# Kernel optimization log

Hardware: AMD Instinct MI355X
Metric: run time of the kernel (lower is better)

## Reference

```python
import jax, jax.numpy as jnp
import numpy as np
from jax import lax

B, H, W, CIN, COUT, K, SDIM = 8, 256, 256, 128, 128, 3, 512


def setup_inputs() -> dict:
    key = jax.random.key(0)
    k1, k2, k3, k4, k5 = jax.random.split(key, 5)
    return {
        "x": jax.random.normal(k1, (B, H, W, CIN), dtype=jnp.float32),
        "style": jax.random.normal(k2, (B, SDIM), dtype=jnp.float32),
        "kernel": jax.random.normal(k3, (K, K, CIN, COUT), dtype=jnp.float32),
        "w_mod": jax.random.normal(k4, (SDIM, CIN), dtype=jnp.float32) / np.sqrt(SDIM),
        "b_mod": jnp.zeros((CIN,), dtype=jnp.float32),
        "noise_strength": jnp.zeros((1,), dtype=jnp.float32),
        "bias": jnp.zeros((COUT,), dtype=jnp.float32),
        "noise": jax.random.normal(k5, (B, H, W, 1), dtype=jnp.float32),
    }


def reference(x, style, kernel, w_mod, b_mod, noise_strength, bias, noise):
    kh, kw, cin, cout = kernel.shape
    # equalized-lr runtime coefficient
    he_std = 1.0 / jnp.sqrt(jnp.asarray(kh * kw * cin, jnp.float32))
    w = kernel * he_std  # [kh,kw,cin,cout]
    # style modulation (Dense with zero constant bias) + 1
    s = style @ w_mod + b_mod + 1.0  # [B, cin]
    # demodulate=True: normalize by global max-abs of style (as in source)
    s = s * (1.0 / jnp.max(jnp.abs(s)))
    # NOTE: source uses style[0] only -> single shared modulated weight
    w = w * s[0][None, None, :, None]
    d = lax.rsqrt(jnp.sum(jnp.square(w), axis=(0, 1, 2)) + 1e-8)  # [cout]
    w = w * d[None, None, None, :]
    # plain conv branch: NHWC, stride 1, SAME padding
    y = lax.conv_general_dilated(
        x, w, window_strides=(1, 1), padding="SAME",
        dimension_numbers=("NHWC", "HWIO", "NHWC"))
    # noise injection (noise_strength is zero-init, kept for faithfulness)
    y = y + noise * (noise_strength / 2.0)
    y = y + bias
    # lrelu(0.2) * sqrt(2)
    y = jnp.where(y >= 0, y, 0.2 * y) * jnp.sqrt(jnp.asarray(2.0, y.dtype))
    return y
```

## Files before the change

kernel.cpp:

```cpp
#include <hip/hip_runtime.h>
#include <hip/hip_bf16.h>

#define H 256
#define W 256
#define CIN 128
#define COUT 128
#define BATCH 8
#define LDA 136

typedef float f32x4 __attribute__((ext_vector_type(4)));
typedef short bf16x8 __attribute__((ext_vector_type(8)));

static __device__ __forceinline__ unsigned short f2bf(float f) {
    unsigned int x = __float_as_uint(f);
    unsigned int r = (x + 0x7fffu + ((x >> 16) & 1u)) >> 16;
    return (unsigned short)r;
}

__global__ __launch_bounds__(1024) void prep_kernel(
    const float* __restrict__ style, const float* __restrict__ kern,
    const float* __restrict__ w_mod, const float* __restrict__ b_mod,
    unsigned short* __restrict__ wprep)
{
    __shared__ float sbuf[1024];
    __shared__ float scaleArr[CIN];
    __shared__ float dArr[COUT];
    const int t = threadIdx.x;
    const int b = t >> 7;
    const int c = t & 127;

    float acc = 0.f;
    const float4* st4 = (const float4*)(style + b * 512);
    for (int k4 = 0; k4 < 128; ++k4) {
        float4 s4 = st4[k4];
        int k = k4 * 4;
        acc += s4.x * w_mod[(k + 0) * CIN + c];
        acc += s4.y * w_mod[(k + 1) * CIN + c];
        acc += s4.z * w_mod[(k + 2) * CIN + c];
        acc += s4.w * w_mod[(k + 3) * CIN + c];
    }
    float sval = acc + b_mod[c] + 1.0f;

    sbuf[t] = fabsf(sval);
    __syncthreads();
    for (int off = 512; off > 0; off >>= 1) {
        if (t < off) sbuf[t] = fmaxf(sbuf[t], sbuf[t + off]);
        __syncthreads();
    }
    float invmax = 1.0f / sbuf[0];
    const float he_std = 1.0f / sqrtf(1152.0f);
    if (t < CIN) scaleArr[t] = sval * invmax * he_std;
    __syncthreads();

    {
        const int co = t & 127;
        const int slice = t >> 7;
        float ss = 0.f;
        for (int j = 0; j < 144; ++j) {
            int i = slice * 144 + j;
            int ci = i & 127;
            float wv = kern[i * 128 + co] * scaleArr[ci];
            ss += wv * wv;
        }
        sbuf[t] = ss;
        __syncthreads();
        if (t < 128) {
            float sum = 0.f;
            for (int sl = 0; sl < 8; ++sl) sum += sbuf[sl * 128 + t];
            dArr[t] = rsqrtf(sum + 1e-8f);
        }
        __syncthreads();
    }

    for (int u = t; u < 9 * 4 * 8 * 64; u += 1024) {
        int lane  = u & 63;
        int ntile = (u >> 6) & 7;
        int kc    = (u >> 9) & 3;
        int kk    = u >> 11;
        int co  = ntile * 16 + (lane & 15);
        int cib = kc * 32 + (lane >> 4) * 8;
        float dv = dArr[co];
        unsigned int packed[4];
        for (int jp = 0; jp < 4; ++jp) {
            int ci0 = cib + jp * 2;
            float w0 = kern[(kk * 128 + ci0)     * 128 + co] * scaleArr[ci0]     * dv;
            float w1 = kern[(kk * 128 + ci0 + 1) * 128 + co] * scaleArr[ci0 + 1] * dv;
            packed[jp] = (unsigned int)f2bf(w0) | ((unsigned int)f2bf(w1) << 16);
        }
        ((uint4*)wprep)[u] = make_uint4(packed[0], packed[1], packed[2], packed[3]);
    }
}

__global__ __launch_bounds__(256) void conv_kernel(
    const float* __restrict__ x, const unsigned short* __restrict__ wprep,
    const float* __restrict__ noise_strength, const float* __restrict__ bias,
    const float* __restrict__ noise, float* __restrict__ out)
{
    __shared__ unsigned short ldsA[130 * LDA];
    const int tid  = threadIdx.x;
    const int lane = tid & 63;
    const int wave = tid >> 6;
    const int wm = wave & 1;
    const int wn = wave >> 1;
    const int wt = blockIdx.x;
    const int h  = blockIdx.y;
    const int b  = blockIdx.z;
    const int wstart = wt * 128;

    f32x4 acc[4][4];
    const f32x4 zero = {0.f, 0.f, 0.f, 0.f};
    for (int i = 0; i < 4; ++i)
        for (int j = 0; j < 4; ++j) acc[i][j] = zero;

    for (int kh = 0; kh < 3; ++kh) {
        __syncthreads();
        const int hImg = h + kh - 1;
        const bool rowValid = (hImg >= 0) && (hImg < H);
        const float* rowPtr = x + ((size_t)(b * H + hImg) * W) * CIN;
        for (int idx = tid; idx < 130 * 32; idx += 256) {
            int p  = idx >> 5;
            int c4 = idx & 31;
            int wImg = wstart - 1 + p;
            float4 v = make_float4(0.f, 0.f, 0.f, 0.f);
            if (rowValid && (unsigned)wImg < (unsigned)W)
                v = *(const float4*)(rowPtr + (size_t)wImg * CIN + c4 * 4);
            ushort4 u;
            u.x = f2bf(v.x); u.y = f2bf(v.y); u.z = f2bf(v.z); u.w = f2bf(v.w);
            *(ushort4*)&ldsA[p * LDA + c4 * 4] = u;
        }
        __syncthreads();

        #pragma unroll
        for (int kw = 0; kw < 3; ++kw) {
            const int kk = kh * 3 + kw;
            #pragma unroll
            for (int kc = 0; kc < 4; ++kc) {
                bf16x8 bfrag[4], afrag[4];
                const bf16x8* bptr = (const bf16x8*)wprep +
                                     (((kk * 4 + kc) * 8 + wn * 4) * 64 + lane);
                #pragma unroll
                for (int j = 0; j < 4; ++j) bfrag[j] = bptr[j * 64];
                const int ka = kc * 32 + (lane >> 4) * 8;
                #pragma unroll
                for (int i = 0; i < 4; ++i) {
                    int m = wm * 64 + i * 16 + (lane & 15) + kw;
                    afrag[i] = *(const bf16x8*)&ldsA[m * LDA + ka];
                }
                #pragma unroll
                for (int i = 0; i < 4; ++i)
                    #pragma unroll
                    for (int j = 0; j < 4; ++j)
                        acc[i][j] = __builtin_amdgcn_mfma_f32_16x16x32_bf16(
                            afrag[i], bfrag[j], acc[i][j], 0, 0, 0);
            }
        }
    }

    const float ns  = noise_strength[0] * 0.5f;
    const float RT2 = 1.41421356237309515f;
    const size_t pixBase = ((size_t)(b * H + h) * W) + wstart;
    #pragma unroll
    for (int i = 0; i < 4; ++i) {
        const int mbase = wm * 64 + i * 16 + ((lane >> 4) << 2);
        #pragma unroll
        for (int r = 0; r < 4; ++r) {
            const size_t pix = pixBase + (mbase + r);
            const float nz = noise[pix] * ns;
            #pragma unroll
            for (int j = 0; j < 4; ++j) {
                const int col = wn * 64 + j * 16 + (lane & 15);
                float v = acc[i][j][r] + nz + bias[col];
                v = (v >= 0.f ? v : 0.2f * v) * RT2;
                out[pix * COUT + col] = v;
            }
        }
    }
}

extern "C" void kernel_launch(void* const* d_in, const int* in_sizes, int n_in,
                              void* d_out, int out_size, void* d_ws, size_t ws_size,
                              hipStream_t stream) {
    const float* x              = (const float*)d_in[0];
    const float* style          = (const float*)d_in[1];
    const float* kern           = (const float*)d_in[2];
    const float* w_mod          = (const float*)d_in[3];
    const float* b_mod          = (const float*)d_in[4];
    const float* noise_strength = (const float*)d_in[5];
    const float* bias           = (const float*)d_in[6];
    const float* noise          = (const float*)d_in[7];
    float* out = (float*)d_out;
    unsigned short* wprep = (unsigned short*)d_ws;

    hipLaunchKernelGGL(prep_kernel, dim3(1), dim3(1024), 0, stream,
                       style, kern, w_mod, b_mod, wprep);
    hipLaunchKernelGGL(conv_kernel, dim3(2, 256, 8), dim3(256), 0, stream,
                       x, wprep, noise_strength, bias, noise, out);
}
```

Baseline: 744.3 us.

## Split weight prep into parallel kernels and load conv A fragments directly from global

The single-block weight prep kernel becomes three kernels: a style-scale kernel, a per-tap sum-of-squares kernel that reduces with atomics, and a 72-block packing kernel, so weight preparation is no longer serialized in one block. The conv kernel drops its LDS staging and barriers. Each wave now reads fp32 input straight from global memory, truncates it to bf16 with perm instructions, and masks out-of-range columns. Rows that fall outside the image are skipped. This trades LDS reuse for redundant global/L2 reads (three kw taps per row), switches round-to-nearest to truncation for the input, and adds a 3-blocks-per-SM launch bound.

```diff
diff --git a/kernel.cpp b/kernel.cpp
--- a/kernel.cpp
+++ b/kernel.cpp
@@ -6,10 +6,14 @@
 #define CIN 128
 #define COUT 128
 #define BATCH 8
-#define LDA 136
 
 typedef float f32x4 __attribute__((ext_vector_type(4)));
 typedef short bf16x8 __attribute__((ext_vector_type(8)));
+typedef unsigned int u32;
+
+#define WPREP_UNITS (9 * 4 * 8 * 64)
+#define SCALE_OFF_F (294912 / 4)
+#define DACC_OFF_F  (295424 / 4)
 
 static __device__ __forceinline__ unsigned short f2bf(float f) {
     unsigned int x = __float_as_uint(f);
@@ -17,14 +21,11 @@
     return (unsigned short)r;
 }
 
-__global__ __launch_bounds__(1024) void prep_kernel(
-    const float* __restrict__ style, const float* __restrict__ kern,
-    const float* __restrict__ w_mod, const float* __restrict__ b_mod,
-    unsigned short* __restrict__ wprep)
+__global__ __launch_bounds__(1024) void prep_a(
+    const float* __restrict__ style, const float* __restrict__ w_mod,
+    const float* __restrict__ b_mod, float* __restrict__ ws_f)
 {
     __shared__ float sbuf[1024];
-    __shared__ float scaleArr[CIN];
-    __shared__ float dArr[COUT];
     const int t = threadIdx.x;
     const int b = t >> 7;
     const int c = t & 127;
@@ -49,54 +50,56 @@
     }
     float invmax = 1.0f / sbuf[0];
     const float he_std = 1.0f / sqrtf(1152.0f);
-    if (t < CIN) scaleArr[t] = sval * invmax * he_std;
+    if (t < 128) ws_f[SCALE_OFF_F + t] = sval * invmax * he_std;
+    if (t >= 128 && t < 256) ws_f[DACC_OFF_F + (t - 128)] = 0.f;
+}
+
+__global__ __launch_bounds__(256) void prep_b(
+    const float* __restrict__ kern, float* __restrict__ ws_f)
+{
+    __shared__ float sbuf[256];
+    const int kk = blockIdx.x;
+    const int t = threadIdx.x;
+    const int co = t & 127;
+    const int half = t >> 7;
+    float ss = 0.f;
+    for (int j = 0; j < 64; ++j) {
+        int ci = half * 64 + j;
+        float wv = kern[(kk * 128 + ci) * 128 + co] * ws_f[SCALE_OFF_F + ci];
+        ss += wv * wv;
+    }
+    sbuf[t] = ss;
     __syncthreads();
-
-    {
-        const int co = t & 127;
-        const int slice = t >> 7;
-        float ss = 0.f;
-        for (int j = 0; j < 144; ++j) {
-            int i = slice * 144 + j;
-            int ci = i & 127;
-            float wv = kern[i * 128 + co] * scaleArr[ci];
-            ss += wv * wv;
-        }
-        sbuf[t] = ss;
-        __syncthreads();
-        if (t < 128) {
-            float sum = 0.f;
-            for (int sl = 0; sl < 8; ++sl) sum += sbuf[sl * 128 + t];
-            dArr[t] = rsqrtf(sum + 1e-8f);
-        }
-        __syncthreads();
-    }
-
-    for (int u = t; u < 9 * 4 * 8 * 64; u += 1024) {
-        int lane  = u & 63;
-        int ntile = (u >> 6) & 7;
-        int kc    = (u >> 9) & 3;
-        int kk    = u >> 11;
-        int co  = ntile * 16 + (lane & 15);
-        int cib = kc * 32 + (lane >> 4) * 8;
-        float dv = dArr[co];
-        unsigned int packed[4];
-        for (int jp = 0; jp < 4; ++jp) {
-            int ci0 = cib + jp * 2;
-            float w0 = kern[(kk * 128 + ci0)     * 128 + co] * scaleArr[ci0]     * dv;
-            float w1 = kern[(kk * 128 + ci0 + 1) * 128 + co] * scaleArr[ci0 + 1] * dv;
-            packed[jp] = (unsigned int)f2bf(w0) | ((unsigned int)f2bf(w1) << 16);
-        }
-        ((uint4*)wprep)[u] = make_uint4(packed[0], packed[1], packed[2], packed[3]);
-    }
-}
-
-__global__ __launch_bounds__(256) void conv_kernel(
+    if (t < 128) atomicAdd(&ws_f[DACC_OFF_F + t], sbuf[t] + sbuf[t + 128]);
+}
+
+__global__ __launch_bounds__(256) void prep_c(
+    const float* __restrict__ kern, const float* __restrict__ ws_f,
+    unsigned short* __restrict__ wprep)
+{
+    const int u = blockIdx.x * 256 + threadIdx.x;
+    int lane  = u & 63;
+    int ntile = (u >> 6) & 7;
+    int kc    = (u >> 9) & 3;
+    int kk    = u >> 11;
+    int co  = ntile * 16 + (lane & 15);
+    int cib = kc * 32 + (lane >> 4) * 8;
+    float dv = rsqrtf(ws_f[DACC_OFF_F + co] + 1e-8f);
+    unsigned int packed[4];
+    for (int jp = 0; jp < 4; ++jp) {
+        int ci0 = cib + jp * 2;
+        float w0 = kern[(kk * 128 + ci0)     * 128 + co] * ws_f[SCALE_OFF_F + ci0]     * dv;
+        float w1 = kern[(kk * 128 + ci0 + 1) * 128 + co] * ws_f[SCALE_OFF_F + ci0 + 1] * dv;
+        packed[jp] = (unsigned int)f2bf(w0) | ((unsigned int)f2bf(w1) << 16);
+    }
+    ((uint4*)wprep)[u] = make_uint4(packed[0], packed[1], packed[2], packed[3]);
+}
+
+__global__ __launch_bounds__(256, 3) void conv_kernel(
     const float* __restrict__ x, const unsigned short* __restrict__ wprep,
     const float* __restrict__ noise_strength, const float* __restrict__ bias,
     const float* __restrict__ noise, float* __restrict__ out)
 {
-    __shared__ unsigned short ldsA[130 * LDA];
     const int tid  = threadIdx.x;
     const int lane = tid & 63;
     const int wave = tid >> 6;
@@ -109,42 +112,52 @@
 
     f32x4 acc[4][4];
     const f32x4 zero = {0.f, 0.f, 0.f, 0.f};
+    #pragma unroll
     for (int i = 0; i < 4; ++i)
+        #pragma unroll
         for (int j = 0; j < 4; ++j) acc[i][j] = zero;
 
+    int aoff[3][4];
+    u32 amask[3][4];
+    #pragma unroll
+    for (int kw = 0; kw < 3; ++kw)
+        #pragma unroll
+        for (int i = 0; i < 4; ++i) {
+            int wImg = wstart + wm * 64 + i * 16 + (lane & 15) + kw - 1;
+            amask[kw][i] = ((unsigned)wImg < (unsigned)W) ? 0xFFFFFFFFu : 0u;
+            int wC = min(max(wImg, 0), W - 1);
+            aoff[kw][i] = wC * CIN + (lane >> 4) * 8;
+        }
+
+    const bf16x8* __restrict__ wf = (const bf16x8*)wprep;
+    const int bvoff = wn * 4 * 64 + lane;
+
     for (int kh = 0; kh < 3; ++kh) {
-        __syncthreads();
         const int hImg = h + kh - 1;
-        const bool rowValid = (hImg >= 0) && (hImg < H);
-        const float* rowPtr = x + ((size_t)(b * H + hImg) * W) * CIN;
-        for (int idx = tid; idx < 130 * 32; idx += 256) {
-            int p  = idx >> 5;
-            int c4 = idx & 31;
-            int wImg = wstart - 1 + p;
-            float4 v = make_float4(0.f, 0.f, 0.f, 0.f);
-            if (rowValid && (unsigned)wImg < (unsigned)W)
-                v = *(const float4*)(rowPtr + (size_t)wImg * CIN + c4 * 4);
-            ushort4 u;
-            u.x = f2bf(v.x); u.y = f2bf(v.y); u.z = f2bf(v.z); u.w = f2bf(v.w);
-            *(ushort4*)&ldsA[p * LDA + c4 * 4] = u;
-        }
-        __syncthreads();
-
-        #pragma unroll
-        for (int kw = 0; kw < 3; ++kw) {
-            const int kk = kh * 3 + kw;
+        if ((unsigned)hImg >= (unsigned)H) continue;
+        const float* __restrict__ rowPtr = x + ((size_t)(b * H + hImg) * W) * CIN;
+        #pragma unroll
+        for (int kc = 0; kc < 4; ++kc) {
             #pragma unroll
-            for (int kc = 0; kc < 4; ++kc) {
-                bf16x8 bfrag[4], afrag[4];
-                const bf16x8* bptr = (const bf16x8*)wprep +
-                                     (((kk * 4 + kc) * 8 + wn * 4) * 64 + lane);
+            for (int kw = 0; kw < 3; ++kw) {
+                const int kk = kh * 3 + kw;
+                bf16x8 bfrag[4];
+                const bf16x8* bp = wf + ((kk * 4 + kc) * 8) * 64 + bvoff;
                 #pragma unroll
-                for (int j = 0; j < 4; ++j) bfrag[j] = bptr[j * 64];
-                const int ka = kc * 32 + (lane >> 4) * 8;
+                for (int j = 0; j < 4; ++j) bfrag[j] = bp[j * 64];
+                bf16x8 afrag[4];
                 #pragma unroll
                 for (int i = 0; i < 4; ++i) {
-                    int m = wm * 64 + i * 16 + (lane & 15) + kw;
-                    afrag[i] = *(const bf16x8*)&ldsA[m * LDA + ka];
+                    const float* pA = rowPtr + aoff[kw][i] + kc * 32;
+                    f32x4 a0 = *(const f32x4*)pA;
+                    f32x4 a1 = *(const f32x4*)(pA + 4);
+                    u32 m = amask[kw][i];
+                    union { u32 u[4]; bf16x8 v; } cv;
+                    cv.u[0] = __builtin_amdgcn_perm(__float_as_uint(a0.y), __float_as_uint(a0.x), 0x07060302u) & m;
+                    cv.u[1] = __builtin_amdgcn_perm(__float_as_uint(a0.w), __float_as_uint(a0.z), 0x07060302u) & m;
+                    cv.u[2] = __builtin_amdgcn_perm(__float_as_uint(a1.y), __float_as_uint(a1.x), 0x07060302u) & m;
+                    cv.u[3] = __builtin_amdgcn_perm(__float_as_uint(a1.w), __float_as_uint(a1.z), 0x07060302u) & m;
+                    afrag[i] = cv.v;
                 }
                 #pragma unroll
                 for (int i = 0; i < 4; ++i)
@@ -190,9 +203,11 @@
     const float* noise          = (const float*)d_in[7];
     float* out = (float*)d_out;
     unsigned short* wprep = (unsigned short*)d_ws;
-
-    hipLaunchKernelGGL(prep_kernel, dim3(1), dim3(1024), 0, stream,
-                       style, kern, w_mod, b_mod, wprep);
+    float* ws_f = (float*)d_ws;
+
+    hipLaunchKernelGGL(prep_a, dim3(1), dim3(1024), 0, stream, style, w_mod, b_mod, ws_f);
+    hipLaunchKernelGGL(prep_b, dim3(9), dim3(256), 0, stream, kern, ws_f);
+    hipLaunchKernelGGL(prep_c, dim3(72), dim3(256), 0, stream, kern, ws_f, wprep);
     hipLaunchKernelGGL(conv_kernel, dim3(2, 256, 8), dim3(256), 0, stream,
                        x, wprep, noise_strength, bias, noise, out);
 }
```

Result: slower. 1.068 ms (+43.4%).
